# Kernel tuning notes

Measured on AMD Instinct MI355X. Metric: run time of the kernel, lower is better.

The kernel has to match this reference:

```python
import jax, jax.numpy as jnp
import numpy as np

B, S, D, A = 8, 4096, 128, 128


def _pos_encoding(seq_len, dim):
    # sin/cos positional encoding, same construction as the torch buffer
    pos = np.arange(seq_len, dtype=np.float32)[:, None]
    div = np.exp(np.arange(0, dim, 2, dtype=np.float32) * (-np.log(10000.0) / dim))
    pe = np.zeros((seq_len, dim), dtype=np.float32)
    pe[:, 0::2] = np.sin(pos * div)
    pe[:, 1::2] = np.cos(pos * div)
    return jnp.asarray(pe)


def setup_inputs() -> dict:
    key = jax.random.key(0)
    ks = jax.random.split(key, 7)
    sc = 1.0 / np.sqrt(D)
    return {
        "x": jax.random.normal(ks[0], (B, S, D), dtype=jnp.float32),
        "Wq": jax.random.normal(ks[1], (D, A), dtype=jnp.float32) * sc,
        "bq": jnp.zeros((A,), dtype=jnp.float32),
        "Wk": jax.random.normal(ks[2], (D, A), dtype=jnp.float32) * sc,
        "bk": jnp.zeros((A,), dtype=jnp.float32),
        "Wv": jax.random.normal(ks[3], (D, A), dtype=jnp.float32) * sc,
        "bv": jnp.zeros((A,), dtype=jnp.float32),
    }


def reference(x, Wq, bq, Wk, bk, Wv, bv):
    b, s, d = x.shape
    pe = _pos_encoding(s, d)  # [S, D]
    xp = x + pe[None]  # broadcast add of positional encoding
    q = xp @ Wq + bq  # [B, S, A]
    k = xp @ Wk + bk
    v = xp @ Wv + bv
    scale = 1.0 / jnp.sqrt(jnp.asarray(Wq.shape[1], dtype=jnp.float32))
    scores = jnp.einsum("bsa,bta->bst", q, k) * scale  # [B, S, S]
    weights = jax.nn.softmax(scores, axis=-1)
    out = jnp.einsum("bst,bta->bsa", weights, v)  # [B, S, A]
    return out
```

## Files before the change

### kernel.cpp

```cpp
#include <hip/hip_runtime.h>

#define BB 8
#define SS 4096
#define DD 128

typedef __attribute__((ext_vector_type(8))) short v8s;
typedef __attribute__((ext_vector_type(4))) short v4s;
typedef __attribute__((ext_vector_type(4))) float v4f;
typedef __attribute__((ext_vector_type(16))) float v16f;

__device__ __forceinline__ unsigned short f2bf(float f) {
    unsigned int u = __float_as_uint(f);
    u += 0x7fffu + ((u >> 16) & 1u);
    return (unsigned short)(u >> 16);
}
__device__ __forceinline__ float bf2f(unsigned short s) {
    return __uint_as_float(((unsigned int)s) << 16);
}
__device__ __forceinline__ unsigned int pk_bf16(float a, float b) {
    unsigned int ua = __float_as_uint(a) + 0x8000u;
    unsigned int ub = __float_as_uint(b) + 0x8000u;
    return __builtin_amdgcn_perm(ub, ua, 0x07060302u);
}

#if !defined(__HIP_DEVICE_COMPILE__)
#define MFMA16(a, b, c) (c)
#define MFMA32(a, b, c) (c)
#else
#define MFMA16(a, b, c) __builtin_amdgcn_mfma_f32_16x16x32_bf16((a), (b), (c), 0, 0, 0)
#define MFMA32(a, b, c) __builtin_amdgcn_mfma_f32_32x32x16_bf16((a), (b), (c), 0, 0, 0)
#endif

#if !defined(__HIP_DEVICE_COMPILE__)
#define EXP2F(x) exp2f(x)
#elif __has_builtin(__builtin_amdgcn_exp2f)
#define EXP2F(x) __builtin_amdgcn_exp2f(x)
#else
#define EXP2F(x) exp2f(x)
#endif

#define QSCALE 0.12751743f
#define FIXM 24.0f

__global__ __launch_bounds__(256) void prep_w_kernel(
    const float* __restrict__ Wq, const float* __restrict__ Wk,
    const float* __restrict__ Wv, unsigned short* __restrict__ Wt)
{
    int id = blockIdx.x * 256 + threadIdx.x;
    int w = id >> 14;
    int n = (id >> 7) & 127;
    int k = id & 127;
    const float* W = (w == 0) ? Wq : (w == 1) ? Wk : Wv;
    Wt[id] = f2bf(W[k * 128 + n]);
}

__global__ __launch_bounds__(256) void prep_pe_kernel(float* __restrict__ pe)
{
    int id = blockIdx.x * 256 + threadIdx.x;
    int s = id >> 5;
    int d0 = (id & 31) * 4;
    v4f r;
#pragma unroll
    for (int j = 0; j < 4; j += 2) {
        float freq = __expf((float)(d0 + j) * -0.07195578415606394f);
        float arg = (float)s * freq;
        r[j] = __sinf(arg);
        r[j + 1] = __cosf(arg);
    }
    *(v4f*)(pe + (size_t)s * DD + d0) = r;
}

__global__ __launch_bounds__(256, 3) void proj_kernel(
    const float* __restrict__ x, const float* __restrict__ pe,
    const unsigned short* __restrict__ Wt,
    const float* __restrict__ bq, const float* __restrict__ bk,
    const float* __restrict__ bv,
    unsigned short* __restrict__ qo, unsigned short* __restrict__ ko,
    unsigned short* __restrict__ vo)
{
    __shared__ __attribute__((aligned(16))) unsigned short w_lds[128 * 136];
    __shared__ __attribute__((aligned(16))) unsigned short o_lds[9216];

    const int tid = threadIdx.x;
    const int wave = tid >> 6;
    const int lane = tid & 63;
    const int quad = lane >> 4;
    const int l15 = lane & 15;
    const int bid = blockIdx.x;
    const int mat = bid % 3;
    const int rbase = (bid / 3) * 64;

    const unsigned short* Wp = Wt + (mat << 14);
#pragma unroll
    for (int it = 0; it < 8; ++it) {
        int id = it * 256 + tid;
        int n = id >> 4, c8 = id & 15;
        *(v8s*)(w_lds + n * 136 + c8 * 8) = *(const v8s*)(Wp + n * 128 + c8 * 8);
    }

    const int flatrow = rbase + wave * 16 + l15;
    const int srow = flatrow & 4095;
    v8s af[4];
#pragma unroll
    for (int kc = 0; kc < 4; ++kc) {
        const int kbase = kc * 32 + quad * 8;
        const v4f* xp = (const v4f*)(x + (size_t)flatrow * DD + kbase);
        const v4f* pp = (const v4f*)(pe + (size_t)srow * DD + kbase);
        v4f x0 = xp[0], x1 = xp[1], p0 = pp[0], p1 = pp[1];
        v8s a;
#pragma unroll
        for (int j = 0; j < 4; ++j) a[j] = (short)f2bf(x0[j] + p0[j]);
#pragma unroll
        for (int j = 0; j < 4; ++j) a[4 + j] = (short)f2bf(x1[j] + p1[j]);
        af[kc] = a;
    }

    const float* bias = (mat == 0) ? bq : (mat == 1) ? bk : bv;
    __syncthreads();

#pragma unroll
    for (int nb = 0; nb < 8; ++nb) {
        const int col = nb * 16 + l15;
        v4f acc = {0.f, 0.f, 0.f, 0.f};
#pragma unroll
        for (int kc = 0; kc < 4; ++kc) {
            v8s bf = *(const v8s*)(w_lds + col * 136 + kc * 32 + quad * 8);
            acc = MFMA16(af[kc], bf, acc);
        }
        float bval = bias[col];
#pragma unroll
        for (int reg = 0; reg < 4; ++reg) {
            int lr = wave * 16 + quad * 4 + reg;
            float val = acc[reg] + bval;
            if (mat == 0) {
                o_lds[lr * 136 + col] = f2bf(val * QSCALE);
            } else if (mat == 1) {
                o_lds[lr * 136 + col] = f2bf(val);
            } else {
                o_lds[col * 72 + lr] = f2bf(val);
            }
        }
    }
    __syncthreads();

    if (mat <= 1) {
        unsigned short* outp = (mat == 0) ? qo : ko;
#pragma unroll
        for (int it = 0; it < 4; ++it) {
            int id = it * 256 + tid;
            int r = id >> 4, c8 = id & 15;
            *(v8s*)(outp + (size_t)(rbase + r) * DD + c8 * 8) =
                *(const v8s*)(o_lds + r * 136 + c8 * 8);
        }
    } else {
        const int b0 = rbase >> 12, s0 = rbase & 4095;
#pragma unroll
        for (int it = 0; it < 4; ++it) {
            int id = it * 256 + tid;
            int a = id >> 3, c = id & 7;
            *(v8s*)(vo + ((size_t)(b0 * 128 + a)) * SS + s0 + c * 8) =
                *(const v8s*)(o_lds + a * 72 + c * 8);
        }
    }
}

#define KT 32
#define HKEYS 2048
#define NT (HKEYS / KT)
__global__ __launch_bounds__(256, 2) void flash_kernel(
    const unsigned short* __restrict__ qg,
    const unsigned short* __restrict__ kg,
    const unsigned short* __restrict__ vg,
    float* __restrict__ out,
    unsigned short* __restrict__ o2,
    float* __restrict__ statl)
{
    __shared__ __attribute__((aligned(16))) unsigned short k_lds[2][KT * 128];
    __shared__ __attribute__((aligned(16))) unsigned short v_lds[2][128 * KT];

    const int tid = threadIdx.x;
    const int wave = tid >> 6;
    const int lane = tid & 63;
    const int hi = lane >> 5;
    const int l31 = lane & 31;
    const int bid = blockIdx.x;
    const int b = bid & 7;
    const int half = (bid >> 3) & 1;
    const int qt = bid >> 4;
    const int qbase = qt * 128 + wave * 32;

    const size_t qrow = (size_t)(b * SS + qbase + l31) * DD;
    v8s qf[8];
#pragma unroll
    for (int kc = 0; kc < 8; ++kc)
        qf[kc] = *(const v8s*)(qg + qrow + kc * 16 + hi * 8);

    v16f o[4];
#pragma unroll
    for (int fg = 0; fg < 4; ++fg)
#pragma unroll
        for (int r = 0; r < 16; ++r) o[fg][r] = 0.f;
    float lrow = 0.f;

    const unsigned short* kb = kg + (size_t)b * SS * DD + (size_t)half * HKEYS * DD;
    const unsigned short* vb = vg + (size_t)b * DD * SS + half * HKEYS;

    const int kr_r = tid >> 4, kr_c = tid & 15;
    const int va = tid >> 2, vc8 = tid & 3;
    v8s kr[2], vr[2];

    auto load_tile = [&](int t) {
        const unsigned short* kp = kb + (size_t)t * KT * DD;
        const unsigned short* vp = vb + t * KT;
#pragma unroll
        for (int it = 0; it < 2; ++it) {
            kr[it] = *(const v8s*)(kp + (size_t)(kr_r + it * 16) * DD + kr_c * 8);
            vr[it] = *(const v8s*)(vp + (size_t)(va + it * 64) * SS + vc8 * 8);
        }
    };
    auto store_tile = [&](int p) {
#pragma unroll
        for (int it = 0; it < 2; ++it) {
            int r = kr_r + it * 16;
            *(v8s*)(&k_lds[p][r * 128 + ((kr_c ^ (r & 7)) << 3)]) = kr[it];
            int a = va + it * 64;
            v4s lo = {vr[it][0], vr[it][1], vr[it][2], vr[it][3]};
            v4s hv = {vr[it][4], vr[it][5], vr[it][6], vr[it][7]};
            int cc = vc8 >> 1, h = vc8 & 1;
            int sw = (a & 3) ^ ((a >> 2) & 1);
            *(v4s*)(&v_lds[p][a * 32 + (((cc ^ sw) << 3) + h * 4)]) = lo;
            *(v4s*)(&v_lds[p][a * 32 + ((((cc + 2) ^ sw) << 3) + h * 4)]) = hv;
        }
    };
    auto compute = [&](int p) {
        v16f s;
#pragma unroll
        for (int r = 0; r < 16; ++r) s[r] = -FIXM;
#pragma unroll
        for (int kc = 0; kc < 8; ++kc) {
            v8s af = *(const v8s*)(&k_lds[p][l31 * 128 +
                                   (((kc * 2 + hi) ^ (l31 & 7)) << 3)]);
            s = MFMA32(af, qf[kc], s);
        }
        float e[16];
#pragma unroll
        for (int r = 0; r < 16; ++r) {
            e[r] = EXP2F(s[r]);
            lrow += e[r];
        }
        union { v8s v[2]; unsigned int u[8]; } P;
#pragma unroll
        for (int g = 0; g < 2; ++g)
#pragma unroll
            for (int m = 0; m < 4; ++m)
                P.u[g * 4 + m] = pk_bf16(e[2 * m + 8 * g], e[2 * m + 8 * g + 1]);
#pragma unroll
        for (int fg = 0; fg < 4; ++fg) {
            int row = fg * 32 + l31;
            int sw = (row & 3) ^ ((row >> 2) & 1);
#pragma unroll
            for (int g = 0; g < 2; ++g) {
                v8s bf = *(const v8s*)(&v_lds[p][row * 32 +
                                       (((2 * hi + g) ^ sw) << 3)]);
                o[fg] = MFMA32(P.v[g], bf, o[fg]);
            }
        }
    };

    load_tile(0);
    store_tile(0);
    load_tile(1);
    __syncthreads();
#pragma unroll 1
    for (int kt = 0; kt < NT; kt += 2) {
        store_tile(1);
        if (kt + 2 < NT) load_tile(kt + 2);
        compute(0);
        __syncthreads();
        if (kt + 2 < NT) {
            store_tile(0);
            if (kt + 3 < NT) load_tile(kt + 3);
        }
        compute(1);
        __syncthreads();
    }

    lrow += __shfl_xor(lrow, 32, 64);
    if (lane < 32)
        statl[half * (BB * SS) + b * SS + qbase + l31] = lrow;
#pragma unroll
    for (int fg = 0; fg < 4; ++fg)
#pragma unroll
        for (int r = 0; r < 16; ++r) {
            int qr = (r & 3) + 8 * (r >> 2) + 4 * hi;
            size_t idx = (size_t)(b * SS + qbase + qr) * DD + fg * 32 + l31;
            if (half == 0) out[idx] = o[fg][r];
            else           o2[idx] = f2bf(o[fg][r]);
        }
}

__global__ __launch_bounds__(256) void combine_kernel(
    float* __restrict__ out, const unsigned short* __restrict__ o2,
    const float* __restrict__ statl)
{
    int id = blockIdx.x * 256 + threadIdx.x;
    int row = id >> 5;
    int c = (id & 31) * 4;
    float l1 = statl[row], l2 = statl[BB * SS + row];
    float inv = 1.0f / (l1 + l2);
    size_t base = (size_t)row * DD + c;
    v4f o1 = *(v4f*)(out + base);
    v4s p2 = *(const v4s*)(o2 + base);
    v4f r;
#pragma unroll
    for (int j = 0; j < 4; ++j)
        r[j] = (o1[j] + bf2f((unsigned short)p2[j])) * inv;
    *(v4f*)(out + base) = r;
}

extern "C" void kernel_launch(void* const* d_in, const int* in_sizes, int n_in,
                              void* d_out, int out_size, void* d_ws, size_t ws_size,
                              hipStream_t stream)
{
    const float* x  = (const float*)d_in[0];
    const float* Wq = (const float*)d_in[1];
    const float* bq = (const float*)d_in[2];
    const float* Wk = (const float*)d_in[3];
    const float* bk = (const float*)d_in[4];
    const float* Wv = (const float*)d_in[5];
    const float* bv = (const float*)d_in[6];
    float* out = (float*)d_out;

    unsigned short* Wt = (unsigned short*)d_ws;
    unsigned short* q  = Wt + 49152;
    unsigned short* k  = q + (size_t)BB * SS * DD;
    unsigned short* vT = k + (size_t)BB * SS * DD;
    unsigned short* O2 = vT + (size_t)BB * SS * DD;
    float* statl = (float*)(O2 + (size_t)BB * SS * DD);
    float* pe    = statl + 2 * BB * SS;

    hipLaunchKernelGGL(prep_w_kernel, dim3(192), dim3(256), 0, stream, Wq, Wk, Wv, Wt);
    hipLaunchKernelGGL(prep_pe_kernel, dim3(512), dim3(256), 0, stream, pe);
    hipLaunchKernelGGL(proj_kernel, dim3(BB * SS / 64 * 3), dim3(256), 0, stream,
                       x, pe, Wt, bq, bk, bv, q, k, vT);
    hipLaunchKernelGGL(flash_kernel, dim3(SS / 128 * 2 * BB), dim3(256), 0, stream,
                       q, k, vT, out, O2, statl);
    hipLaunchKernelGGL(combine_kernel, dim3(BB * SS * DD / 4 / 256), dim3(256), 0, stream,
                       out, O2, statl);
}
```

Baseline: 181.1 us.

## Merge split-K halves in one block via LDS, drop combine kernel

The flash kernel now runs both key halves in one 512-thread block. Each half accumulates its own partial output, and the row sums are now computed with an MFMA against a ones vector instead of scalar adds. The second half's partial output and sums go through the reused K/V LDS buffers, and the first half normalizes and writes the final fp32 output directly. This removes the bf16 O2 round-trip through global memory, the stats buffer and the separate combine kernel launch, and the two prep kernels are merged into one launch. In exchange, blocks are larger with 64KB of LDS plus an extra sync at the end, which may lower occupancy.

New measurement: 178.0 us. No clear change (-1.7%).

```diff
diff --git a/kernel.cpp b/kernel.cpp
--- a/kernel.cpp
+++ b/kernel.cpp
@@ -13,9 +13,6 @@
     unsigned int u = __float_as_uint(f);
     u += 0x7fffu + ((u >> 16) & 1u);
     return (unsigned short)(u >> 16);
-}
-__device__ __forceinline__ float bf2f(unsigned short s) {
-    return __uint_as_float(((unsigned int)s) << 16);
 }
 __device__ __forceinline__ unsigned int pk_bf16(float a, float b) {
     unsigned int ua = __float_as_uint(a) + 0x8000u;
@@ -42,32 +39,34 @@
 #define QSCALE 0.12751743f
 #define FIXM 24.0f
 
-__global__ __launch_bounds__(256) void prep_w_kernel(
+__global__ __launch_bounds__(256) void prep_kernel(
     const float* __restrict__ Wq, const float* __restrict__ Wk,
-    const float* __restrict__ Wv, unsigned short* __restrict__ Wt)
+    const float* __restrict__ Wv, unsigned short* __restrict__ Wt,
+    float* __restrict__ pe)
 {
-    int id = blockIdx.x * 256 + threadIdx.x;
-    int w = id >> 14;
-    int n = (id >> 7) & 127;
-    int k = id & 127;
-    const float* W = (w == 0) ? Wq : (w == 1) ? Wk : Wv;
-    Wt[id] = f2bf(W[k * 128 + n]);
-}
-
-__global__ __launch_bounds__(256) void prep_pe_kernel(float* __restrict__ pe)
-{
-    int id = blockIdx.x * 256 + threadIdx.x;
-    int s = id >> 5;
-    int d0 = (id & 31) * 4;
-    v4f r;
-#pragma unroll
-    for (int j = 0; j < 4; j += 2) {
-        float freq = __expf((float)(d0 + j) * -0.07195578415606394f);
-        float arg = (float)s * freq;
-        r[j] = __sinf(arg);
-        r[j + 1] = __cosf(arg);
-    }
-    *(v4f*)(pe + (size_t)s * DD + d0) = r;
+    int bid = blockIdx.x;
+    int tid = threadIdx.x;
+    if (bid < 192) {
+        int id = bid * 256 + tid;
+        int w = id >> 14;
+        int n = (id >> 7) & 127;
+        int k = id & 127;
+        const float* W = (w == 0) ? Wq : (w == 1) ? Wk : Wv;
+        Wt[id] = f2bf(W[k * 128 + n]);
+    } else {
+        int id = (bid - 192) * 256 + tid;
+        int s = id >> 5;
+        int d0 = (id & 31) * 4;
+        v4f r;
+#pragma unroll
+        for (int j = 0; j < 4; j += 2) {
+            float freq = __expf((float)(d0 + j) * -0.07195578415606394f);
+            float arg = (float)s * freq;
+            r[j] = __sinf(arg);
+            r[j + 1] = __cosf(arg);
+        }
+        *(v4f*)(pe + (size_t)s * DD + d0) = r;
+    }
 }
 
 __global__ __launch_bounds__(256, 3) void proj_kernel(
@@ -167,29 +166,29 @@
 #define KT 32
 #define HKEYS 2048
 #define NT (HKEYS / KT)
-__global__ __launch_bounds__(256, 2) void flash_kernel(
+__global__ __launch_bounds__(512, 2) void flash_kernel(
     const unsigned short* __restrict__ qg,
     const unsigned short* __restrict__ kg,
     const unsigned short* __restrict__ vg,
-    float* __restrict__ out,
-    unsigned short* __restrict__ o2,
-    float* __restrict__ statl)
+    float* __restrict__ out)
 {
-    __shared__ __attribute__((aligned(16))) unsigned short k_lds[2][KT * 128];
-    __shared__ __attribute__((aligned(16))) unsigned short v_lds[2][128 * KT];
+    __shared__ __attribute__((aligned(16))) unsigned short k_lds[2][2][4096];
+    __shared__ __attribute__((aligned(16))) unsigned short v_lds[2][2][4096];
+    __shared__ float xl[128];
 
     const int tid = threadIdx.x;
     const int wave = tid >> 6;
     const int lane = tid & 63;
     const int hi = lane >> 5;
     const int l31 = lane & 31;
+    const int half = tid >> 8;
+    const int qs = wave & 3;
     const int bid = blockIdx.x;
     const int b = bid & 7;
-    const int half = (bid >> 3) & 1;
-    const int qt = bid >> 4;
-    const int qbase = qt * 128 + wave * 32;
-
-    const size_t qrow = (size_t)(b * SS + qbase + l31) * DD;
+    const int qt = bid >> 3;
+    const int qbase = qt * 128;
+
+    const size_t qrow = (size_t)(b * SS + qbase + qs * 32 + l31) * DD;
     v8s qf[8];
 #pragma unroll
     for (int kc = 0; kc < 8; ++kc)
@@ -200,13 +199,20 @@
     for (int fg = 0; fg < 4; ++fg)
 #pragma unroll
         for (int r = 0; r < 16; ++r) o[fg][r] = 0.f;
-    float lrow = 0.f;
+    v16f lacc;
+#pragma unroll
+    for (int r = 0; r < 16; ++r) lacc[r] = 0.f;
+
+    v8s ones;
+#pragma unroll
+    for (int j = 0; j < 8; ++j) ones[j] = (short)0x3F80;
 
     const unsigned short* kb = kg + (size_t)b * SS * DD + (size_t)half * HKEYS * DD;
     const unsigned short* vb = vg + (size_t)b * DD * SS + half * HKEYS;
 
-    const int kr_r = tid >> 4, kr_c = tid & 15;
-    const int va = tid >> 2, vc8 = tid & 3;
+    const int tid2 = tid & 255;
+    const int kr_r = tid2 >> 4, kr_c = tid2 & 15;
+    const int va = tid2 >> 2, vc8 = tid2 & 3;
     v8s kr[2], vr[2];
 
     auto load_tile = [&](int t) {
@@ -222,14 +228,14 @@
 #pragma unroll
         for (int it = 0; it < 2; ++it) {
             int r = kr_r + it * 16;
-            *(v8s*)(&k_lds[p][r * 128 + ((kr_c ^ (r & 7)) << 3)]) = kr[it];
+            *(v8s*)(&k_lds[half][p][r * 128 + ((kr_c ^ (r & 7)) << 3)]) = kr[it];
             int a = va + it * 64;
             v4s lo = {vr[it][0], vr[it][1], vr[it][2], vr[it][3]};
             v4s hv = {vr[it][4], vr[it][5], vr[it][6], vr[it][7]};
             int cc = vc8 >> 1, h = vc8 & 1;
             int sw = (a & 3) ^ ((a >> 2) & 1);
-            *(v4s*)(&v_lds[p][a * 32 + (((cc ^ sw) << 3) + h * 4)]) = lo;
-            *(v4s*)(&v_lds[p][a * 32 + ((((cc + 2) ^ sw) << 3) + h * 4)]) = hv;
+            *(v4s*)(&v_lds[half][p][a * 32 + (((cc ^ sw) << 3) + h * 4)]) = lo;
+            *(v4s*)(&v_lds[half][p][a * 32 + ((((cc + 2) ^ sw) << 3) + h * 4)]) = hv;
         }
     };
     auto compute = [&](int p) {
@@ -238,16 +244,13 @@
         for (int r = 0; r < 16; ++r) s[r] = -FIXM;
 #pragma unroll
         for (int kc = 0; kc < 8; ++kc) {
-            v8s af = *(const v8s*)(&k_lds[p][l31 * 128 +
+            v8s af = *(const v8s*)(&k_lds[half][p][l31 * 128 +
                                    (((kc * 2 + hi) ^ (l31 & 7)) << 3)]);
             s = MFMA32(af, qf[kc], s);
         }
         float e[16];
 #pragma unroll
-        for (int r = 0; r < 16; ++r) {
-            e[r] = EXP2F(s[r]);
-            lrow += e[r];
-        }
+        for (int r = 0; r < 16; ++r) e[r] = EXP2F(s[r]);
         union { v8s v[2]; unsigned int u[8]; } P;
 #pragma unroll
         for (int g = 0; g < 2; ++g)
@@ -255,12 +258,13 @@
             for (int m = 0; m < 4; ++m)
                 P.u[g * 4 + m] = pk_bf16(e[2 * m + 8 * g], e[2 * m + 8 * g + 1]);
 #pragma unroll
-        for (int fg = 0; fg < 4; ++fg) {
-            int row = fg * 32 + l31;
-            int sw = (row & 3) ^ ((row >> 2) & 1);
-#pragma unroll
-            for (int g = 0; g < 2; ++g) {
-                v8s bf = *(const v8s*)(&v_lds[p][row * 32 +
+        for (int g = 0; g < 2; ++g) {
+            lacc = MFMA32(P.v[g], ones, lacc);
+#pragma unroll
+            for (int fg = 0; fg < 4; ++fg) {
+                int row = fg * 32 + l31;
+                int sw = (row & 3) ^ ((row >> 2) & 1);
+                v8s bf = *(const v8s*)(&v_lds[half][p][row * 32 +
                                        (((2 * hi + g) ^ sw) << 3)]);
                 o[fg] = MFMA32(P.v[g], bf, o[fg]);
             }
@@ -285,37 +289,56 @@
         __syncthreads();
     }
 
-    lrow += __shfl_xor(lrow, 32, 64);
-    if (lane < 32)
-        statl[half * (BB * SS) + b * SS + qbase + l31] = lrow;
-#pragma unroll
-    for (int fg = 0; fg < 4; ++fg)
+    float* kf = (float*)&k_lds[0][0][0];
+    float* vf = (float*)&v_lds[0][0][0];
+    float* xch = (qs < 2) ? (kf + qs * 4096) : (vf + (qs - 2) * 4096);
+
+    if (half == 1) {
+#pragma unroll
+        for (int fg = 0; fg < 4; ++fg) {
+            v4f* base = (v4f*)(xch + fg * 1024 + lane * 16);
+#pragma unroll
+            for (int c = 0; c < 4; ++c) {
+                v4f t = {o[fg][c * 4 + 0], o[fg][c * 4 + 1],
+                         o[fg][c * 4 + 2], o[fg][c * 4 + 3]};
+                base[c ^ (lane & 3)] = t;
+            }
+        }
+        if (l31 == 0) {
+#pragma unroll
+            for (int r = 0; r < 16; ++r) {
+                int qr = (r & 3) + 8 * (r >> 2) + 4 * hi;
+                xl[qs * 32 + qr] = lacc[r];
+            }
+        }
+    }
+    __syncthreads();
+    if (half == 0) {
+#pragma unroll
+        for (int fg = 0; fg < 4; ++fg) {
+            const v4f* base = (const v4f*)(xch + fg * 1024 + lane * 16);
+#pragma unroll
+            for (int c = 0; c < 4; ++c) {
+                v4f t = base[c ^ (lane & 3)];
+#pragma unroll
+                for (int j = 0; j < 4; ++j) o[fg][c * 4 + j] += t[j];
+            }
+        }
+        float ir[16];
 #pragma unroll
         for (int r = 0; r < 16; ++r) {
             int qr = (r & 3) + 8 * (r >> 2) + 4 * hi;
-            size_t idx = (size_t)(b * SS + qbase + qr) * DD + fg * 32 + l31;
-            if (half == 0) out[idx] = o[fg][r];
-            else           o2[idx] = f2bf(o[fg][r]);
-        }
-}
-
-__global__ __launch_bounds__(256) void combine_kernel(
-    float* __restrict__ out, const unsigned short* __restrict__ o2,
-    const float* __restrict__ statl)
-{
-    int id = blockIdx.x * 256 + threadIdx.x;
-    int row = id >> 5;
-    int c = (id & 31) * 4;
-    float l1 = statl[row], l2 = statl[BB * SS + row];
-    float inv = 1.0f / (l1 + l2);
-    size_t base = (size_t)row * DD + c;
-    v4f o1 = *(v4f*)(out + base);
-    v4s p2 = *(const v4s*)(o2 + base);
-    v4f r;
-#pragma unroll
-    for (int j = 0; j < 4; ++j)
-        r[j] = (o1[j] + bf2f((unsigned short)p2[j])) * inv;
-    *(v4f*)(out + base) = r;
+            ir[r] = 1.0f / (lacc[r] + xl[qs * 32 + qr]);
+        }
+#pragma unroll
+        for (int fg = 0; fg < 4; ++fg)
+#pragma unroll
+            for (int r = 0; r < 16; ++r) {
+                int qr = (r & 3) + 8 * (r >> 2) + 4 * hi;
+                out[(size_t)(b * SS + qbase + qs * 32 + qr) * DD + fg * 32 + l31] =
+                    o[fg][r] * ir[r];
+            }
+    }
 }
 
 extern "C" void kernel_launch(void* const* d_in, const int* in_sizes, int n_in,
@@ -335,16 +358,12 @@
     unsigned short* q  = Wt + 49152;
     unsigned short* k  = q + (size_t)BB * SS * DD;
     unsigned short* vT = k + (size_t)BB * SS * DD;
-    unsigned short* O2 = vT + (size_t)BB * SS * DD;
-    float* statl = (float*)(O2 + (size_t)BB * SS * DD);
-    float* pe    = statl + 2 * BB * SS;
-
-    hipLaunchKernelGGL(prep_w_kernel, dim3(192), dim3(256), 0, stream, Wq, Wk, Wv, Wt);
-    hipLaunchKernelGGL(prep_pe_kernel, dim3(512), dim3(256), 0, stream, pe);
+    float* pe = (float*)(vT + (size_t)BB * SS * DD);
+
+    hipLaunchKernelGGL(prep_kernel, dim3(704), dim3(256), 0, stream,
+                       Wq, Wk, Wv, Wt, pe);
     hipLaunchKernelGGL(proj_kernel, dim3(BB * SS / 64 * 3), dim3(256), 0, stream,
                        x, pe, Wt, bq, bk, bv, q, k, vT);
-    hipLaunchKernelGGL(flash_kernel, dim3(SS / 128 * 2 * BB), dim3(256), 0, stream,
-                       q, k, vT, out, O2, statl);
-    hipLaunchKernelGGL(combine_kernel, dim3(BB * SS * DD / 4 / 256), dim3(256), 0, stream,
-                       out, O2, statl);
-}
+    hipLaunchKernelGGL(flash_kernel, dim3(BB * SS / 128), dim3(512), 0, stream,
+                       q, k, vT, out);
+}
```
